# Kernel optimization log

Hardware: AMD Instinct MI355X
Metric: run time of the kernel (lower is better)

## Reference

```python
import jax, jax.numpy as jnp
import numpy as np

B, N, E, H = 16, 1024, 1024, 16  # batch must equal num_heads due to the 'hbkd' einsum in the original
D = E // H


def setup_inputs() -> dict:
    key = jax.random.key(0)
    ks = jax.random.split(key, 9)
    s = 0.02
    return {
        "x": jax.random.normal(ks[0], (B, N, E), dtype=jnp.float32),
        "Wq": jax.random.normal(ks[1], (E, E), dtype=jnp.float32) * s,
        "bq": jax.random.normal(ks[2], (E,), dtype=jnp.float32) * s,
        "Wk": jax.random.normal(ks[3], (E, E), dtype=jnp.float32) * s,
        "bk": jax.random.normal(ks[4], (E,), dtype=jnp.float32) * s,
        "Wv": jax.random.normal(ks[5], (E, E), dtype=jnp.float32) * s,
        "bv": jax.random.normal(ks[6], (E,), dtype=jnp.float32) * s,
        "Wp": jax.random.normal(ks[7], (E, E), dtype=jnp.float32) * s,
        "bp": jax.random.normal(ks[8], (E,), dtype=jnp.float32) * s,
    }


def _split_heads(t):  # [b, n, (h d)] -> [b, h, n, d]
    b, n, e = t.shape
    return t.reshape(b, n, H, D).transpose(0, 2, 1, 3)


def reference(x, Wq, bq, Wk, bk, Wv, bv, Wp, bp):
    q = _split_heads(x @ Wq.T + bq)  # [b, h, n, d]
    k = _split_heads(x @ Wk.T + bk)
    v = _split_heads(x @ Wv.T + bv)
    # Faithful to original: K is contracted with its batch/head axes SWAPPED ('hbkd').
    energy = jnp.einsum('bhqd,hbkd->bhqk', q, k)  # [b, h, n, n]
    # Faithful: softmax over the HEAD axis (dim=1), scale applied AFTER softmax.
    scale = E ** 0.5
    att = jax.nn.softmax(energy, axis=1) / scale
    # dropout rate is 0.0 -> identity
    o = jnp.einsum('bhal,bhlv->bhav', att, v)  # [b, h, n, d]
    o = o.transpose(0, 2, 1, 3).reshape(B, N, E)  # [b, n, (h d)]
    return o @ Wp.T + bp
```

## Files before the change

### kernel.cpp

```cpp
#include <hip/hip_runtime.h>
#include <hip/hip_bf16.h>

#define DEVI __device__ __forceinline__

typedef float f32x4 __attribute__((ext_vector_type(4)));
typedef short bf16x8 __attribute__((ext_vector_type(8)));
typedef unsigned short u16x4 __attribute__((ext_vector_type(4)));


DEVI unsigned short f2bf(float f) {
  union { float f; unsigned u; } v; v.f = f;
  unsigned r = v.u + 0x7fffu + ((v.u >> 16) & 1u);
  return (unsigned short)(r >> 16);
}

DEVI float fexp2(float x) {
#if __has_builtin(__builtin_amdgcn_exp2f)
  return __builtin_amdgcn_exp2f(x);
#else
  return exp2f(x);
#endif
}

DEVI float frcp(float x) {
#if __has_builtin(__builtin_amdgcn_rcpf)
  return __builtin_amdgcn_rcpf(x);
#else
  return 1.0f / x;
#endif
}

DEVI unsigned cvtpk(float a, float b) {
  unsigned r;
  asm("v_cvt_pk_bf16_f32 %0, %1, %2" : "=v"(r) : "v"(a), "v"(b));
  return r;
}

DEVI void gload_lds16(const unsigned short* g, unsigned short* l) {
  __builtin_amdgcn_global_load_lds(
      (const __attribute__((address_space(1))) void*)g,
      (__attribute__((address_space(3))) void*)l, 16, 0, 0);
}

__global__ void cvt_kernel(const float* __restrict__ s, unsigned short* __restrict__ d, int n4) {
  int i = blockIdx.x * blockDim.x + threadIdx.x;
  const int st = gridDim.x * blockDim.x;
  for (; i < n4; i += st) {
    const float4 v = reinterpret_cast<const float4*>(s)[i];
    u16x4 o;
    o[0] = f2bf(v.x); o[1] = f2bf(v.y); o[2] = f2bf(v.z); o[3] = f2bf(v.w);
    reinterpret_cast<u16x4*>(d)[i] = o;
  }
}

DEVI void gemm_tile(const unsigned short* __restrict__ A,
                    const unsigned short* __restrict__ Bw,
                    int m0, int n0,
                    unsigned short* lsA, unsigned short* lsB,
                    f32x4 acc[4][4]) {
  const int tid = threadIdx.x;
  const int w = tid >> 6, l = tid & 63, lg = l >> 4, lr = l & 15;
  const int wr = w >> 1, wc = w & 1;
  for (int kt = 0; kt < 1024; kt += 64) {
#pragma unroll
    for (int i = 0; i < 4; i++) {
      const int c = i * 256 + tid;
      const int row = c >> 3, col = (c & 7) * 8;
      gload_lds16(&A[(m0 + row) * 1024 + kt + col], &lsA[(i * 256 + w * 64) * 8]);
      gload_lds16(&Bw[(n0 + row) * 1024 + kt + col], &lsB[(i * 256 + w * 64) * 8]);
    }
    __syncthreads();
#pragma unroll
    for (int ks = 0; ks < 2; ks++) {
      bf16x8 af[4], bf_[4];
#pragma unroll
      for (int fi = 0; fi < 4; fi++) af[fi] = *(const bf16x8*)&lsA[(wr * 64 + fi * 16 + lr) * 64 + ks * 32 + lg * 8];
#pragma unroll
      for (int fj = 0; fj < 4; fj++) bf_[fj] = *(const bf16x8*)&lsB[(wc * 64 + fj * 16 + lr) * 64 + ks * 32 + lg * 8];
#pragma unroll
      for (int fi = 0; fi < 4; fi++)
#pragma unroll
        for (int fj = 0; fj < 4; fj++)
          acc[fi][fj] = __builtin_amdgcn_mfma_f32_16x16x32_bf16(af[fi], bf_[fj], acc[fi][fj], 0, 0, 0);
    }
    __syncthreads();
  }
}

__global__ __launch_bounds__(256, 2) void proj_qkv(
    const unsigned short* __restrict__ X, const unsigned short* __restrict__ W3,
    const float* __restrict__ bq, const float* __restrict__ bk, const float* __restrict__ bv,
    unsigned short* __restrict__ outq, unsigned short* __restrict__ outk, unsigned short* __restrict__ outv) {
  __shared__ unsigned short lsA[128 * 64];
  __shared__ unsigned short lsB[128 * 64];
  const int z = blockIdx.z;
  const int m0 = blockIdx.x * 128, n0 = blockIdx.y * 128;
  const unsigned short* Bw = W3 + z * 1048576;
  f32x4 acc[4][4];
  const f32x4 z4 = {0.f, 0.f, 0.f, 0.f};
#pragma unroll
  for (int i = 0; i < 4; i++)
#pragma unroll
    for (int j = 0; j < 4; j++) acc[i][j] = z4;
  gemm_tile(X, Bw, m0, n0, lsA, lsB, acc);

  const int tid = threadIdx.x;
  const int w = tid >> 6, l = tid & 63, lg = l >> 4, lr = l & 15, wr = w >> 1, wc = w & 1;
  const float* bias = (z == 0) ? bq : ((z == 1) ? bk : bv);
  const float SC = 1.4426950408889634f;
#pragma unroll
  for (int fi = 0; fi < 4; fi++) {
    const int mb = m0 + wr * 64 + fi * 16 + lg * 4;
#pragma unroll
    for (int fj = 0; fj < 4; fj++) {
      const int ncol = n0 + wc * 64 + fj * 16 + lr;
      const float bsv = bias[ncol];
      const int h = ncol >> 6, d = ncol & 63;
      if (z == 0) {
        const int ks = d >> 5, lgq = (d >> 3) & 3, eq = d & 7;
#pragma unroll
        for (int r = 0; r < 4; r++) {
          const int m = mb + r;
          const int bb = m >> 10, nr = m & 1023;
          const int nt = nr >> 4, lrq = nr & 15;
          const int idx = (((bb * 64 + nt) * 32 + h * 2 + ks) * 64 + lgq * 16 + lrq) * 8 + eq;
          outq[idx] = f2bf((acc[fi][fj][r] + bsv) * SC);
        }
      } else if (z == 1) {
        const int ks = d >> 5, lhi = ((d >> 3) & 3) * 16, eq = d & 7;
#pragma unroll
        for (int r = 0; r < 4; r++) {
          const int m = mb + r;
          const int n = m & 1023, bx = m >> 10;
          const int lane = lhi + (n & 15);
          const int idx = ((((h * 64 + (n >> 4)) * 16 + bx) * 2 + ks) * 64 + lane) * 8 + eq;
          outk[idx] = f2bf(acc[fi][fj][r] + bsv);
        }
      } else {
        const int dt = d >> 4, lrv = d & 15;
        const int bb = mb >> 10, n = mb & 1023;
        const int kc = n >> 5, lgv = (n >> 3) & 3, ev = n & 7;
        u16x4 pk;
#pragma unroll
        for (int r = 0; r < 4; r++) pk[r] = f2bf(acc[fi][fj][r] + bsv);
        const int idx0 = ((((bb * 16 + h) * 32 + kc) * 4 + dt) * 64 + lgv * 16 + lrv) * 8 + ev;
        *(u16x4*)&outv[idx0] = pk;
      }
    }
  }
}

__global__ __launch_bounds__(256, 2) void proj_out(
    const unsigned short* __restrict__ A, const unsigned short* __restrict__ Wp,
    const float* __restrict__ bias, float* __restrict__ out) {
  __shared__ unsigned short lsA[128 * 64];
  __shared__ unsigned short lsB[128 * 64];
  const int m0 = blockIdx.x * 128, n0 = blockIdx.y * 128;
  f32x4 acc[4][4];
  const f32x4 z4 = {0.f, 0.f, 0.f, 0.f};
#pragma unroll
  for (int i = 0; i < 4; i++)
#pragma unroll
    for (int j = 0; j < 4; j++) acc[i][j] = z4;
  gemm_tile(A, Wp, m0, n0, lsA, lsB, acc);
  const int tid = threadIdx.x;
  const int w = tid >> 6, l = tid & 63, lg = l >> 4, lr = l & 15, wr = w >> 1, wc = w & 1;
#pragma unroll
  for (int fi = 0; fi < 4; fi++) {
    const int mb = m0 + wr * 64 + fi * 16 + lg * 4;
#pragma unroll
    for (int fj = 0; fj < 4; fj++) {
      const int ncol = n0 + wc * 64 + fj * 16 + lr;
      const float bsv = bias[ncol];
#pragma unroll
      for (int r = 0; r < 4; r++) out[(mb + r) * 1024 + ncol] = acc[fi][fj][r] + bsv;
    }
  }
}

__global__ __launch_bounds__(1024, 4) void attn4(
    const unsigned short* __restrict__ Q2,
    const unsigned short* __restrict__ K2,
    const unsigned short* __restrict__ V2,
    unsigned short* __restrict__ O) {
  __shared__ unsigned short qlds[32768];
  __shared__ unsigned short abuf[32768];

  const int tid = threadIdx.x;
  const int w = tid >> 6, l = tid & 63;
  const int lr = l & 15, lg = l >> 4;
  const int bid = blockIdx.x;
  const int swz = (bid & 7) * 64 + (bid >> 3);
  const int b = swz >> 5, qt32 = swz & 31;
  const int ksub = w & 3, hq = w >> 2;

  {
    const unsigned short* qsrc = Q2 + (size_t)(b * 64 + qt32 * 2) * 16384 + tid * 8;
    unsigned short* qdst = qlds + tid * 8;
#pragma unroll
    for (int r = 0; r < 4; r++) gload_lds16(qsrc + r * 8192, qdst + r * 8192);
  }

  const int kpart = ksub * 16 + lg * 4;
  const int wswz = (lr & 7) << 3;

  const f32x4 z4 = {0.f, 0.f, 0.f, 0.f};
  f32x4 oacc[2][4];
#pragma unroll
  for (int qt = 0; qt < 2; qt++)
#pragma unroll
    for (int dt = 0; dt < 4; dt++) oacc[qt][dt] = z4;

  __syncthreads();

#pragma unroll 1
  for (int it = 0; it < 16; it++) {
    int qo = 0;
    asm volatile("" : "+v"(qo));
    const int kt = it * 4 + ksub;
    const unsigned short* kp = K2 + (size_t)(b * 64 + kt) * 16384 + l * 8;

    f32x4 e[4][2];
#pragma unroll
    for (int hl = 0; hl < 4; hl++) {
      const int h = hq * 4 + hl;
      bf16x8 k0 = *(const bf16x8*)(kp + (h * 2 + 0) * 512);
      bf16x8 k1 = *(const bf16x8*)(kp + (h * 2 + 1) * 512);
#pragma unroll
      for (int qh = 0; qh < 2; qh++) {
        bf16x8 q0 = *(const bf16x8*)((const char*)qlds + qo + (qh * 32 + h * 2 + 0) * 1024 + l * 16);
        bf16x8 q1 = *(const bf16x8*)((const char*)qlds + qo + (qh * 32 + h * 2 + 1) * 1024 + l * 16);
        f32x4 t = __builtin_amdgcn_mfma_f32_16x16x32_bf16(k0, q0, z4, 0, 0, 0);
        t = __builtin_amdgcn_mfma_f32_16x16x32_bf16(k1, q1, t, 0, 0, 0);
        t[0] = fexp2(t[0]); t[1] = fexp2(t[1]); t[2] = fexp2(t[2]); t[3] = fexp2(t[3]);
        e[hl][qh] = t;
      }
    }
    f32x4 s0 = (e[0][0] + e[1][0]) + (e[2][0] + e[3][0]);
    f32x4 s1 = (e[0][1] + e[1][1]) + (e[2][1] + e[3][1]);
    __syncthreads();
    *(f32x4*)((char*)abuf + (((ksub * 4 + hq) * 2 + 0) * 64 + l) * 16) = s0;
    *(f32x4*)((char*)abuf + (((ksub * 4 + hq) * 2 + 1) * 64 + l) * 16) = s1;
    __syncthreads();
#pragma unroll
    for (int p = 1; p < 4; p++) {
      const int hqp = hq ^ p;
      s0 += *(const f32x4*)((char*)abuf + (((ksub * 4 + hqp) * 2 + 0) * 64 + l) * 16);
      s1 += *(const f32x4*)((char*)abuf + (((ksub * 4 + hqp) * 2 + 1) * 64 + l) * 16);
    }
    f32x4 inv0, inv1;
    inv0[0] = frcp(s0[0]) * 0.03125f; inv0[1] = frcp(s0[1]) * 0.03125f;
    inv0[2] = frcp(s0[2]) * 0.03125f; inv0[3] = frcp(s0[3]) * 0.03125f;
    inv1[0] = frcp(s1[0]) * 0.03125f; inv1[1] = frcp(s1[1]) * 0.03125f;
    inv1[2] = frcp(s1[2]) * 0.03125f; inv1[3] = frcp(s1[3]) * 0.03125f;
    __syncthreads();
#pragma unroll
    for (int hl = 0; hl < 4; hl++) {
      const int h = hq * 4 + hl;
#pragma unroll
      for (int qh = 0; qh < 2; qh++) {
        f32x4 v = e[hl][qh] * (qh ? inv1 : inv0);
        uint2 pk;
        pk.x = cvtpk(v[0], v[1]);
        pk.y = cvtpk(v[2], v[3]);
        const int q = qh * 16 + lr;
        *(uint2*)((char*)abuf + h * 4096 + q * 128 + ((kpart ^ wswz) << 1)) = pk;
      }
    }
    __syncthreads();
    const int kc0 = it * 2;
    const char* vbp = (const char*)V2 + (size_t)(((b * 16 + w) * 32 + kc0) * 4) * 1024 + l * 16;
    bf16x8 vb[2][4];
#pragma unroll
    for (int kst = 0; kst < 2; kst++)
#pragma unroll
      for (int dt = 0; dt < 4; dt++)
        vb[kst][dt] = *(const bf16x8*)(vbp + (kst * 4 + dt) * 1024);
    bf16x8 pa[2][2];
#pragma unroll
    for (int qt = 0; qt < 2; qt++)
#pragma unroll
      for (int kst = 0; kst < 2; kst++)
        pa[qt][kst] = *(const bf16x8*)((const char*)abuf + w * 4096 + qt * 2048 + lr * 128 +
                                       (((kst * 4 + lg) ^ (lr & 7)) << 4));
#pragma unroll
    for (int qt = 0; qt < 2; qt++)
#pragma unroll
      for (int kst = 0; kst < 2; kst++)
#pragma unroll
        for (int dt = 0; dt < 4; dt++)
          oacc[qt][dt] = __builtin_amdgcn_mfma_f32_16x16x32_bf16(pa[qt][kst], vb[kst][dt], oacc[qt][dt], 0, 0, 0);
  }

#pragma unroll
  for (int qt = 0; qt < 2; qt++)
#pragma unroll
    for (int dt = 0; dt < 4; dt++)
#pragma unroll
      for (int r = 0; r < 4; r++) {
        const int n = qt32 * 32 + qt * 16 + lg * 4 + r;
        O[(size_t)(b * 1024 + n) * 1024 + w * 64 + dt * 16 + lr] = f2bf(oacc[qt][dt][r]);
      }
}

extern "C" void kernel_launch(void* const* d_in, const int* in_sizes, int n_in,
                              void* d_out, int out_size, void* d_ws, size_t ws_size,
                              hipStream_t stream) {
  const float* x  = (const float*)d_in[0];
  const float* Wq = (const float*)d_in[1];
  const float* bq = (const float*)d_in[2];
  const float* Wk = (const float*)d_in[3];
  const float* bk = (const float*)d_in[4];
  const float* Wv = (const float*)d_in[5];
  const float* bv = (const float*)d_in[6];
  const float* Wp = (const float*)d_in[7];
  const float* bp = (const float*)d_in[8];

  char* ws = (char*)d_ws;
  unsigned short* xbf  = (unsigned short*)(ws);
  unsigned short* qbf  = (unsigned short*)(ws + 33554432);
  unsigned short* kbf  = (unsigned short*)(ws + 67108864);
  unsigned short* vtbf = (unsigned short*)(ws + 100663296);
  unsigned short* wbf  = (unsigned short*)(ws + 134217728);

  cvt_kernel<<<2048, 256, 0, stream>>>(x, xbf, 4194304);
  cvt_kernel<<<512, 256, 0, stream>>>(Wq, wbf, 262144);
  cvt_kernel<<<512, 256, 0, stream>>>(Wk, wbf + 1048576, 262144);
  cvt_kernel<<<512, 256, 0, stream>>>(Wv, wbf + 2097152, 262144);
  cvt_kernel<<<512, 256, 0, stream>>>(Wp, wbf + 3145728, 262144);

  proj_qkv<<<dim3(128, 8, 3), 256, 0, stream>>>(xbf, wbf, bq, bk, bv, qbf, kbf, vtbf);
  attn4<<<512, 1024, 0, stream>>>(qbf, kbf, vtbf, xbf);
  proj_out<<<dim3(128, 8, 1), 256, 0, stream>>>(xbf, wbf + 3145728, bp, (float*)d_out);
}
```

Baseline: 352.1 us.

## Double-buffer K tiles in registers and cut barriers in attention loop

Replaces the attention kernel with a version that prefetches the next iteration's K fragments into registers (ping-pong kA/kB) while computing the current one. Row-sum reduction moves to a dedicated LDS buffer, so the per-iteration barriers drop from four to two. V loads are issued before the barrier that precedes the PV MFMAs. This is meant to hide global load latency and synchronisation cost, at the price of more registers and extra LDS.

Result: no change. 350.3 us (-0.5%).

```diff
diff --git a/kernel.cpp b/kernel.cpp
--- a/kernel.cpp
+++ b/kernel.cpp
@@ -40,6 +40,12 @@
   __builtin_amdgcn_global_load_lds(
       (const __attribute__((address_space(1))) void*)g,
       (__attribute__((address_space(3))) void*)l, 16, 0, 0);
+}
+
+DEVI void wg_barrier() {
+  asm volatile("s_waitcnt lgkmcnt(0)" ::: "memory");
+  __builtin_amdgcn_s_barrier();
+  __builtin_amdgcn_sched_barrier(0);
 }
 
 __global__ void cvt_kernel(const float* __restrict__ s, unsigned short* __restrict__ d, int n4) {
@@ -178,13 +184,76 @@
   }
 }
 
-__global__ __launch_bounds__(1024, 4) void attn4(
+#define ATTN_BODY(IT, KC, KN)                                                  \
+  {                                                                            \
+    int qo = 0;                                                                \
+    asm volatile("" : "+v"(qo));                                               \
+    f32x4 e[4][2];                                                             \
+    _Pragma("unroll") for (int hl = 0; hl < 4; hl++) {                         \
+      const int h = hq * 4 + hl;                                               \
+      _Pragma("unroll") for (int qh = 0; qh < 2; qh++) {                       \
+        bf16x8 q0 = *(const bf16x8*)((const char*)qlds + qo + (qh * 32 + h * 2 + 0) * 1024 + l * 16); \
+        bf16x8 q1 = *(const bf16x8*)((const char*)qlds + qo + (qh * 32 + h * 2 + 1) * 1024 + l * 16); \
+        f32x4 t = __builtin_amdgcn_mfma_f32_16x16x32_bf16(KC[hl * 2 + 0], q0, z4, 0, 0, 0); \
+        t = __builtin_amdgcn_mfma_f32_16x16x32_bf16(KC[hl * 2 + 1], q1, t, 0, 0, 0); \
+        t[0] = fexp2(t[0]); t[1] = fexp2(t[1]); t[2] = fexp2(t[2]); t[3] = fexp2(t[3]); \
+        e[hl][qh] = t;                                                         \
+      }                                                                        \
+    }                                                                          \
+    {                                                                          \
+      const unsigned short* knp = kroot + (size_t)((((IT) + 1) & 15) * 4) * 16384; \
+      _Pragma("unroll") for (int i = 0; i < 8; i++) KN[i] = *(const bf16x8*)(knp + i * 512); \
+    }                                                                          \
+    f32x4 s0 = (e[0][0] + e[1][0]) + (e[2][0] + e[3][0]);                      \
+    f32x4 s1 = (e[0][1] + e[1][1]) + (e[2][1] + e[3][1]);                      \
+    *(f32x4*)&sumbuf[((ksub * 4 + hq) * 2 + 0) * 256 + l * 4] = s0;            \
+    *(f32x4*)&sumbuf[((ksub * 4 + hq) * 2 + 1) * 256 + l * 4] = s1;            \
+    wg_barrier();                                                              \
+    _Pragma("unroll") for (int p = 1; p < 4; p++) {                            \
+      const int hqp = hq ^ p;                                                  \
+      s0 += *(const f32x4*)&sumbuf[((ksub * 4 + hqp) * 2 + 0) * 256 + l * 4];  \
+      s1 += *(const f32x4*)&sumbuf[((ksub * 4 + hqp) * 2 + 1) * 256 + l * 4];  \
+    }                                                                          \
+    f32x4 inv0, inv1;                                                          \
+    inv0[0] = frcp(s0[0]) * 0.03125f; inv0[1] = frcp(s0[1]) * 0.03125f;        \
+    inv0[2] = frcp(s0[2]) * 0.03125f; inv0[3] = frcp(s0[3]) * 0.03125f;        \
+    inv1[0] = frcp(s1[0]) * 0.03125f; inv1[1] = frcp(s1[1]) * 0.03125f;        \
+    inv1[2] = frcp(s1[2]) * 0.03125f; inv1[3] = frcp(s1[3]) * 0.03125f;        \
+    _Pragma("unroll") for (int hl = 0; hl < 4; hl++) {                         \
+      const int h = hq * 4 + hl;                                               \
+      _Pragma("unroll") for (int qh = 0; qh < 2; qh++) {                       \
+        f32x4 vv = e[hl][qh] * (qh ? inv1 : inv0);                             \
+        uint2 pk;                                                              \
+        pk.x = cvtpk(vv[0], vv[1]);                                            \
+        pk.y = cvtpk(vv[2], vv[3]);                                            \
+        *(uint2*)((char*)abuf + h * 4096 + (qh * 16 + lr) * 128 + ((kpart ^ wswz) << 1)) = pk; \
+      }                                                                        \
+    }                                                                          \
+    {                                                                          \
+      const unsigned short* vbp = vroot + (size_t)((IT) * 2) * 2048;           \
+      _Pragma("unroll") for (int kst = 0; kst < 2; kst++)                      \
+        _Pragma("unroll") for (int dt = 0; dt < 4; dt++)                       \
+          vr[kst * 4 + dt] = *(const bf16x8*)(vbp + kst * 2048 + dt * 512);    \
+    }                                                                          \
+    wg_barrier();                                                              \
+    bf16x8 pa[2][2];                                                           \
+    _Pragma("unroll") for (int qt = 0; qt < 2; qt++)                           \
+      _Pragma("unroll") for (int kst = 0; kst < 2; kst++)                      \
+        pa[qt][kst] = *(const bf16x8*)((const char*)abuf + w * 4096 + qt * 2048 + lr * 128 + (((kst * 4 + lg) ^ (lr & 7)) << 4)); \
+    _Pragma("unroll") for (int qt = 0; qt < 2; qt++)                           \
+      _Pragma("unroll") for (int kst = 0; kst < 2; kst++)                      \
+        _Pragma("unroll") for (int dt = 0; dt < 4; dt++)                       \
+          oacc[qt][dt] = __builtin_amdgcn_mfma_f32_16x16x32_bf16(pa[qt][kst], vr[kst * 4 + dt], oacc[qt][dt], 0, 0, 0); \
+  }
+
+__global__ __launch_bounds__(1024, 4) void attn5(
     const unsigned short* __restrict__ Q2,
     const unsigned short* __restrict__ K2,
     const unsigned short* __restrict__ V2,
     unsigned short* __restrict__ O) {
   __shared__ unsigned short qlds[32768];
   __shared__ unsigned short abuf[32768];
+  __shared__ float sumbuf[8192];
 
   const int tid = threadIdx.x;
   const int w = tid >> 6, l = tid & 63;
@@ -211,85 +280,21 @@
 #pragma unroll
     for (int dt = 0; dt < 4; dt++) oacc[qt][dt] = z4;
 
-  __syncthreads();
+  const unsigned short* kroot = K2 + (size_t)(b * 64 + ksub) * 16384 + hq * 4096 + l * 8;
+  const unsigned short* vroot = V2 + (size_t)((b * 16 + w) * 32) * 2048 + l * 8;
+
+  bf16x8 kA[8], kB[8], vr[8];
+#pragma unroll
+  for (int i = 0; i < 8; i++) kA[i] = *(const bf16x8*)(kroot + i * 512);
+
+  asm volatile("s_waitcnt vmcnt(0) lgkmcnt(0)" ::: "memory");
+  __builtin_amdgcn_s_barrier();
+  __builtin_amdgcn_sched_barrier(0);
 
 #pragma unroll 1
-  for (int it = 0; it < 16; it++) {
-    int qo = 0;
-    asm volatile("" : "+v"(qo));
-    const int kt = it * 4 + ksub;
-    const unsigned short* kp = K2 + (size_t)(b * 64 + kt) * 16384 + l * 8;
-
-    f32x4 e[4][2];
-#pragma unroll
-    for (int hl = 0; hl < 4; hl++) {
-      const int h = hq * 4 + hl;
-      bf16x8 k0 = *(const bf16x8*)(kp + (h * 2 + 0) * 512);
-      bf16x8 k1 = *(const bf16x8*)(kp + (h * 2 + 1) * 512);
-#pragma unroll
-      for (int qh = 0; qh < 2; qh++) {
-        bf16x8 q0 = *(const bf16x8*)((const char*)qlds + qo + (qh * 32 + h * 2 + 0) * 1024 + l * 16);
-        bf16x8 q1 = *(const bf16x8*)((const char*)qlds + qo + (qh * 32 + h * 2 + 1) * 1024 + l * 16);
-        f32x4 t = __builtin_amdgcn_mfma_f32_16x16x32_bf16(k0, q0, z4, 0, 0, 0);
-        t = __builtin_amdgcn_mfma_f32_16x16x32_bf16(k1, q1, t, 0, 0, 0);
-        t[0] = fexp2(t[0]); t[1] = fexp2(t[1]); t[2] = fexp2(t[2]); t[3] = fexp2(t[3]);
-        e[hl][qh] = t;
-      }
-    }
-    f32x4 s0 = (e[0][0] + e[1][0]) + (e[2][0] + e[3][0]);
-    f32x4 s1 = (e[0][1] + e[1][1]) + (e[2][1] + e[3][1]);
-    __syncthreads();
-    *(f32x4*)((char*)abuf + (((ksub * 4 + hq) * 2 + 0) * 64 + l) * 16) = s0;
-    *(f32x4*)((char*)abuf + (((ksub * 4 + hq) * 2 + 1) * 64 + l) * 16) = s1;
-    __syncthreads();
-#pragma unroll
-    for (int p = 1; p < 4; p++) {
-      const int hqp = hq ^ p;
-      s0 += *(const f32x4*)((char*)abuf + (((ksub * 4 + hqp) * 2 + 0) * 64 + l) * 16);
-      s1 += *(const f32x4*)((char*)abuf + (((ksub * 4 + hqp) * 2 + 1) * 64 + l) * 16);
-    }
-    f32x4 inv0, inv1;
-    inv0[0] = frcp(s0[0]) * 0.03125f; inv0[1] = frcp(s0[1]) * 0.03125f;
-    inv0[2] = frcp(s0[2]) * 0.03125f; inv0[3] = frcp(s0[3]) * 0.03125f;
-    inv1[0] = frcp(s1[0]) * 0.03125f; inv1[1] = frcp(s1[1]) * 0.03125f;
-    inv1[2] = frcp(s1[2]) * 0.03125f; inv1[3] = frcp(s1[3]) * 0.03125f;
-    __syncthreads();
-#pragma unroll
-    for (int hl = 0; hl < 4; hl++) {
-      const int h = hq * 4 + hl;
-#pragma unroll
-      for (int qh = 0; qh < 2; qh++) {
-        f32x4 v = e[hl][qh] * (qh ? inv1 : inv0);
-        uint2 pk;
-        pk.x = cvtpk(v[0], v[1]);
-        pk.y = cvtpk(v[2], v[3]);
-        const int q = qh * 16 + lr;
-        *(uint2*)((char*)abuf + h * 4096 + q * 128 + ((kpart ^ wswz) << 1)) = pk;
-      }
-    }
-    __syncthreads();
-    const int kc0 = it * 2;
-    const char* vbp = (const char*)V2 + (size_t)(((b * 16 + w) * 32 + kc0) * 4) * 1024 + l * 16;
-    bf16x8 vb[2][4];
-#pragma unroll
-    for (int kst = 0; kst < 2; kst++)
-#pragma unroll
-      for (int dt = 0; dt < 4; dt++)
-        vb[kst][dt] = *(const bf16x8*)(vbp + (kst * 4 + dt) * 1024);
-    bf16x8 pa[2][2];
-#pragma unroll
-    for (int qt = 0; qt < 2; qt++)
-#pragma unroll
-      for (int kst = 0; kst < 2; kst++)
-        pa[qt][kst] = *(const bf16x8*)((const char*)abuf + w * 4096 + qt * 2048 + lr * 128 +
-                                       (((kst * 4 + lg) ^ (lr & 7)) << 4));
-#pragma unroll
-    for (int qt = 0; qt < 2; qt++)
-#pragma unroll
-      for (int kst = 0; kst < 2; kst++)
-#pragma unroll
-        for (int dt = 0; dt < 4; dt++)
-          oacc[qt][dt] = __builtin_amdgcn_mfma_f32_16x16x32_bf16(pa[qt][kst], vb[kst][dt], oacc[qt][dt], 0, 0, 0);
+  for (int it2 = 0; it2 < 8; it2++) {
+    ATTN_BODY(it2 * 2, kA, kB)
+    ATTN_BODY(it2 * 2 + 1, kB, kA)
   }
 
 #pragma unroll
@@ -330,6 +335,6 @@
   cvt_kernel<<<512, 256, 0, stream>>>(Wp, wbf + 3145728, 262144);
 
   proj_qkv<<<dim3(128, 8, 3), 256, 0, stream>>>(xbf, wbf, bq, bk, bv, qbf, kbf, vtbf);
-  attn4<<<512, 1024, 0, stream>>>(qbf, kbf, vtbf, xbf);
+  attn5<<<512, 1024, 0, stream>>>(qbf, kbf, vtbf, xbf);
   proj_out<<<dim3(128, 8, 1), 256, 0, stream>>>(xbf, wbf + 3145728, bp, (float*)d_out);
 }
```
